# Performance work log

Hardware: AMD Instinct MI355X
Metric: run time of the kernel (lower is better)

The kernel has to match this reference:

```python
import jax, jax.numpy as jnp
import numpy as np

IN = 4096      # in_channels (unpacked)
OUT = 11008    # out_channels
GROUP = 128    # quantization group size
W_BIT = 4
PACK = 32 // W_BIT  # 8 int4 values per int32
N_GROUPS = IN // GROUP
BATCH = 64


def setup_inputs() -> dict:
    key = jax.random.key(0)
    k1, k2, k3, k4 = jax.random.split(key, 4)
    x = jax.random.normal(k1, (BATCH, IN), dtype=jnp.float32)
    # bit-packed int4 weights: 8 nibbles per int32, packed along input dim
    qweight = jax.random.randint(k2, (IN // PACK, OUT), 0, jnp.iinfo(jnp.int32).max, dtype=jnp.int32)
    scales = jax.random.uniform(k3, (N_GROUPS, OUT), dtype=jnp.float32) * 0.01 + 1e-3
    # zero points near mid-range of int4
    zeros = 7.5 + jax.random.uniform(k4, (N_GROUPS, OUT), dtype=jnp.float32) - 0.5
    g_idx = (jnp.arange(IN) // GROUP).astype(jnp.int32)
    return {"x": x, "qweight": qweight, "scales": scales, "zeros": zeros, "g_idx": g_idx}


def unpack_int4(qweight):
    # [IN//8, OUT] int32 -> [IN, OUT] float32 in [0, 15]
    shifts = (jnp.arange(PACK, dtype=jnp.int32) * W_BIT)  # [8]
    nibbles = (qweight[:, None, :] >> shifts[None, :, None]) & 0xF  # [IN//8, 8, OUT]
    return nibbles.reshape(IN, OUT).astype(jnp.float32)


def reference(x, qweight, scales, zeros, g_idx):
    w_int = unpack_int4(qweight)                       # [IN, OUT]
    W = (w_int - zeros[g_idx]) * scales[g_idx]         # group-wise dequant, [IN, OUT]
    return x @ W                                       # [BATCH, OUT]
```

## Files before the change

kernel.cpp:

```cpp
#include <hip/hip_runtime.h>
#include <stdint.h>


#define IN 4096
#define OUT 11008
#define BATCH 64
#define SPLITK 8
#define KSPL (IN / SPLITK)
#define BN 128
#define BK 64
#define NBLK (OUT / BN)
#define LDR 72

typedef __attribute__((ext_vector_type(8))) __bf16 bf16x8;
typedef __attribute__((ext_vector_type(4))) float f32x4;

static __device__ __forceinline__ ushort f2bf(float f) {
  uint32_t u = __float_as_uint(f);
  u += 0x7fff + ((u >> 16) & 1);
  return (ushort)(u >> 16);
}

__global__ void cvt_x_kernel(const float* __restrict__ x, ushort* __restrict__ xbf) {
  int gid = blockIdx.x * blockDim.x + threadIdx.x;
  float4 v = ((const float4*)x)[gid];
  ushort4 o;
  o.x = f2bf(v.x); o.y = f2bf(v.y); o.z = f2bf(v.z); o.w = f2bf(v.w);
  ((ushort4*)xbf)[gid] = o;
}

__global__ __launch_bounds__(256, 2) void mpq_gemm(
    const ushort* __restrict__ xbf,
    const int* __restrict__ qweight,
    const float* __restrict__ scales,
    const float* __restrict__ zeros,
    float* __restrict__ out)
{
  __shared__ ushort At[64 * LDR];
  __shared__ ushort Bt[128 * LDR];

  const int n0 = blockIdx.x * BN;
  const int k0 = blockIdx.y * KSPL;

  const int tid = threadIdx.x;
  const int lane = tid & 63;
  const int w = tid >> 6;
  const int wm = w >> 1, wn = w & 1;
  const int mlane = lane & 15, quad = lane >> 4;

  const int rA = tid >> 2;
  const int kA = (tid & 3) * 16;
  const int rB = tid >> 5;
  const int ncol = tid & 31;

  f32x4 acc[2][4] = {};

  for (int kc = k0; kc < k0 + KSPL; kc += BK) {
    const int g = kc >> 7;

    const uint4* asrc = (const uint4*)(xbf + rA * IN + kc + kA);
    uint4 a0 = asrc[0];
    uint4 a1 = asrc[1];

    int qv[4];
    float sv[4], zv[4];
    const int qrow = (kc >> 3) + rB;
#pragma unroll
    for (int c = 0; c < 4; ++c) {
      int n = ncol + 32 * c;
      qv[c] = qweight[qrow * OUT + n0 + n];
      sv[c] = scales[g * OUT + n0 + n];
      zv[c] = zeros[g * OUT + n0 + n];
    }

    __syncthreads();

    *(uint4*)&At[rA * LDR + kA] = a0;
    *(uint4*)&At[rA * LDR + kA + 8] = a1;

#pragma unroll
    for (int c = 0; c < 4; ++c) {
      const float s = sv[c];
      const float nzs = -zv[c] * s;
      const uint32_t q = (uint32_t)qv[c];
      ushort ob[8];
#pragma unroll
      for (int j = 0; j < 8; ++j) {
        float wf = (float)((q >> (4 * j)) & 0xF);
        ob[j] = f2bf(fmaf(wf, s, nzs));
      }
      *(uint4*)&Bt[(ncol + 32 * c) * LDR + rB * 8] = *(uint4*)ob;
    }

    __syncthreads();

#pragma unroll
    for (int ks = 0; ks < BK; ks += 32) {
      bf16x8 af[2], bfr[4];
#pragma unroll
      for (int i = 0; i < 2; ++i)
        af[i] = *(const bf16x8*)&At[(32 * wm + 16 * i + mlane) * LDR + ks + quad * 8];
#pragma unroll
      for (int j = 0; j < 4; ++j)
        bfr[j] = *(const bf16x8*)&Bt[(64 * wn + 16 * j + mlane) * LDR + ks + quad * 8];
#pragma unroll
      for (int i = 0; i < 2; ++i)
#pragma unroll
        for (int j = 0; j < 4; ++j)
          acc[i][j] = __builtin_amdgcn_mfma_f32_16x16x32_bf16(af[i], bfr[j], acc[i][j], 0, 0, 0);
    }
  }

#pragma unroll
  for (int i = 0; i < 2; ++i) {
    const int mbase = 32 * wm + 16 * i + quad * 4;
#pragma unroll
    for (int j = 0; j < 4; ++j) {
      const int col = n0 + 64 * wn + 16 * j + mlane;
#pragma unroll
      for (int r = 0; r < 4; ++r) {
        atomicAdd(&out[(mbase + r) * OUT + col], acc[i][j][r]);
      }
    }
  }
}

extern "C" void kernel_launch(void* const* d_in, const int* in_sizes, int n_in,
                              void* d_out, int out_size, void* d_ws, size_t ws_size,
                              hipStream_t stream) {
  const float* x = (const float*)d_in[0];
  const int* qweight = (const int*)d_in[1];
  const float* scales = (const float*)d_in[2];
  const float* zeros = (const float*)d_in[3];
  float* out = (float*)d_out;
  ushort* xbf = (ushort*)d_ws;

  hipMemsetAsync(d_out, 0, (size_t)BATCH * OUT * sizeof(float), stream);
  cvt_x_kernel<<<256, 256, 0, stream>>>(x, xbf);
  dim3 grid(NBLK, SPLITK);
  mpq_gemm<<<grid, 256, 0, stream>>>(xbf, qweight, scales, zeros, out);
}
```

Before: 106.0 us.

## Factor dequant out of MFMA via magic-number bf16 nibbles and group row sums

Rewrites the GEMM so int4 nibbles become bf16 directly through a 0x4300 magic-bias trick with no per-element float conversion or LDS staging of B. The per-group scale and zero are applied after the MFMAs, using precomputed per-group row sums of x, and results are folded into a running accumulator. x is pre-packed into MFMA fragment order, and the split-K atomics are replaced by per-split partial buffers plus a separate reduction kernel. This removes dequant ALU work and B shared-memory traffic, at the cost of an extra launch and extra partial-buffer write and read traffic.

```diff
diff --git a/kernel.cpp b/kernel.cpp
--- a/kernel.cpp
+++ b/kernel.cpp
@@ -6,11 +6,9 @@
 #define OUT 11008
 #define BATCH 64
 #define SPLITK 8
-#define KSPL (IN / SPLITK)
+#define KSPL 512
 #define BN 128
-#define BK 64
-#define NBLK (OUT / BN)
-#define LDR 72
+#define GRID_N 86
 
 typedef __attribute__((ext_vector_type(8))) __bf16 bf16x8;
 typedef __attribute__((ext_vector_type(4))) float f32x4;
@@ -20,109 +18,138 @@
   u += 0x7fff + ((u >> 16) & 1);
   return (ushort)(u >> 16);
 }
-
-__global__ void cvt_x_kernel(const float* __restrict__ x, ushort* __restrict__ xbf) {
-  int gid = blockIdx.x * blockDim.x + threadIdx.x;
-  float4 v = ((const float4*)x)[gid];
-  ushort4 o;
-  o.x = f2bf(v.x); o.y = f2bf(v.y); o.z = f2bf(v.z); o.w = f2bf(v.w);
-  ((ushort4*)xbf)[gid] = o;
+static __device__ __forceinline__ float bf2f(ushort h) {
+  return __uint_as_float(((uint32_t)h) << 16);
 }
 
-__global__ __launch_bounds__(256, 2) void mpq_gemm(
+__global__ void cvt_frag_kernel(const float* __restrict__ x,
+                                ushort* __restrict__ xbf,
+                                float* __restrict__ xsum) {
+  const int ks = blockIdx.x;
+  const int i = threadIdx.x >> 6;
+  const int lane = threadIdx.x & 63;
+  const int mlane = lane & 15, quad = lane >> 4;
+  const int m = 16 * i + mlane;
+  const int kb = 32 * ks + 8 * quad;
+  const float4 lo = *(const float4*)&x[m * IN + kb];
+  const float4 hi = *(const float4*)&x[m * IN + kb + 4];
+  ushort o[8];
+  o[0] = f2bf(lo.x); o[1] = f2bf(hi.x);
+  o[2] = f2bf(lo.y); o[3] = f2bf(hi.y);
+  o[4] = f2bf(lo.z); o[5] = f2bf(hi.z);
+  o[6] = f2bf(lo.w); o[7] = f2bf(hi.w);
+  const int flat = (ks * 4 + i) * 64 + lane;
+  *(uint4*)&xbf[flat * 8] = *(uint4*)o;
+  float s = 0.f;
+#pragma unroll
+  for (int j = 0; j < 8; ++j) s += bf2f(o[j]);
+  s += __shfl_xor(s, 16);
+  s += __shfl_xor(s, 32);
+  if (quad == 0) atomicAdd(&xsum[(ks >> 2) * 64 + m], s);
+}
+
+__global__ __launch_bounds__(128, 2) void mpq_gemm(
     const ushort* __restrict__ xbf,
     const int* __restrict__ qweight,
     const float* __restrict__ scales,
     const float* __restrict__ zeros,
-    float* __restrict__ out)
+    const float* __restrict__ xsum,
+    float* __restrict__ P)
 {
-  __shared__ ushort At[64 * LDR];
-  __shared__ ushort Bt[128 * LDR];
+  __shared__ uint4 A_lds[2048];
 
   const int n0 = blockIdx.x * BN;
-  const int k0 = blockIdx.y * KSPL;
-
+  const int sp = blockIdx.y;
+  const int k0 = sp * KSPL;
   const int tid = threadIdx.x;
   const int lane = tid & 63;
   const int w = tid >> 6;
-  const int wm = w >> 1, wn = w & 1;
   const int mlane = lane & 15, quad = lane >> 4;
+  const int ncol = n0 + 64 * w + mlane;
 
-  const int rA = tid >> 2;
-  const int kA = (tid & 3) * 16;
-  const int rB = tid >> 5;
-  const int ncol = tid & 31;
+  f32x4 macc[4][4] = {};
 
-  f32x4 acc[2][4] = {};
+  const uint4* gA = (const uint4*)xbf + (size_t)(k0 / 32) * 256;
 
-  for (int kc = k0; kc < k0 + KSPL; kc += BK) {
-    const int g = kc >> 7;
-
-    const uint4* asrc = (const uint4*)(xbf + rA * IN + kc + kA);
-    uint4 a0 = asrc[0];
-    uint4 a1 = asrc[1];
-
-    int qv[4];
-    float sv[4], zv[4];
-    const int qrow = (kc >> 3) + rB;
+  for (int h = 0; h < 2; ++h) {
+    __syncthreads();
+    const uint4* src = gA + (size_t)h * 8 * 256;
 #pragma unroll
-    for (int c = 0; c < 4; ++c) {
-      int n = ncol + 32 * c;
-      qv[c] = qweight[qrow * OUT + n0 + n];
-      sv[c] = scales[g * OUT + n0 + n];
-      zv[c] = zeros[g * OUT + n0 + n];
-    }
-
+    for (int it = 0; it < 16; ++it)
+      A_lds[tid + 128 * it] = src[tid + 128 * it];
     __syncthreads();
 
-    *(uint4*)&At[rA * LDR + kA] = a0;
-    *(uint4*)&At[rA * LDR + kA + 8] = a1;
-
+    const int qrow0 = k0 / 8 + h * 32;
 #pragma unroll
-    for (int c = 0; c < 4; ++c) {
-      const float s = sv[c];
-      const float nzs = -zv[c] * s;
-      const uint32_t q = (uint32_t)qv[c];
-      ushort ob[8];
+    for (int g2 = 0; g2 < 2; ++g2) {
+      f32x4 gacc[4][4] = {};
 #pragma unroll
-      for (int j = 0; j < 8; ++j) {
-        float wf = (float)((q >> (4 * j)) & 0xF);
-        ob[j] = f2bf(fmaf(wf, s, nzs));
-      }
-      *(uint4*)&Bt[(ncol + 32 * c) * LDR + rB * 8] = *(uint4*)ob;
-    }
-
-    __syncthreads();
-
-#pragma unroll
-    for (int ks = 0; ks < BK; ks += 32) {
-      bf16x8 af[2], bfr[4];
-#pragma unroll
-      for (int i = 0; i < 2; ++i)
-        af[i] = *(const bf16x8*)&At[(32 * wm + 16 * i + mlane) * LDR + ks + quad * 8];
-#pragma unroll
-      for (int j = 0; j < 4; ++j)
-        bfr[j] = *(const bf16x8*)&Bt[(64 * wn + 16 * j + mlane) * LDR + ks + quad * 8];
-#pragma unroll
-      for (int i = 0; i < 2; ++i)
+      for (int ksl = 0; ksl < 4; ++ksl) {
+        const int ks = g2 * 4 + ksl;
+        uint32_t q[4];
+        const int qrow = qrow0 + ks * 4 + quad;
 #pragma unroll
         for (int j = 0; j < 4; ++j)
-          acc[i][j] = __builtin_amdgcn_mfma_f32_16x16x32_bf16(af[i], bfr[j], acc[i][j], 0, 0, 0);
+          q[j] = (uint32_t)qweight[(size_t)qrow * OUT + ncol + 16 * j];
+        bf16x8 af[4];
+#pragma unroll
+        for (int i = 0; i < 4; ++i)
+          af[i] = *(const bf16x8*)&A_lds[(ks * 4 + i) * 64 + lane];
+#pragma unroll
+        for (int j = 0; j < 4; ++j) {
+          uint32_t p[4];
+          p[0] = ( q[j]        & 0x000F000Fu) | 0x43004300u;
+          p[1] = ((q[j] >>  4) & 0x000F000Fu) | 0x43004300u;
+          p[2] = ((q[j] >>  8) & 0x000F000Fu) | 0x43004300u;
+          p[3] = ((q[j] >> 12) & 0x000F000Fu) | 0x43004300u;
+          bf16x8 bfr = *(bf16x8*)p;
+#pragma unroll
+          for (int i = 0; i < 4; ++i)
+            gacc[i][j] = __builtin_amdgcn_mfma_f32_16x16x32_bf16(af[i], bfr, gacc[i][j], 0, 0, 0);
+        }
+      }
+      const int g = (k0 >> 7) + h * 2 + g2;
+      float Sv[4][4];
+#pragma unroll
+      for (int i = 0; i < 4; ++i)
+#pragma unroll
+        for (int r = 0; r < 4; ++r)
+          Sv[i][r] = xsum[g * 64 + 16 * i + 4 * quad + r];
+#pragma unroll
+      for (int j = 0; j < 4; ++j) {
+        const float s = scales[g * OUT + ncol + 16 * j];
+        const float z = zeros[g * OUT + ncol + 16 * j];
+        const float u = s * (128.0f + z);
+#pragma unroll
+        for (int i = 0; i < 4; ++i)
+#pragma unroll
+          for (int r = 0; r < 4; ++r)
+            macc[i][j][r] = fmaf(s, gacc[i][j][r], fmaf(-u, Sv[i][r], macc[i][j][r]));
+      }
     }
   }
 
+  float* Pp = P + (size_t)sp * BATCH * OUT;
 #pragma unroll
-  for (int i = 0; i < 2; ++i) {
-    const int mbase = 32 * wm + 16 * i + quad * 4;
+  for (int i = 0; i < 4; ++i)
 #pragma unroll
-    for (int j = 0; j < 4; ++j) {
-      const int col = n0 + 64 * wn + 16 * j + mlane;
+    for (int r = 0; r < 4; ++r) {
+      const int m = 16 * i + 4 * quad + r;
 #pragma unroll
-      for (int r = 0; r < 4; ++r) {
-        atomicAdd(&out[(mbase + r) * OUT + col], acc[i][j][r]);
-      }
+      for (int j = 0; j < 4; ++j)
+        Pp[(size_t)m * OUT + ncol + 16 * j] = macc[i][j][r];
     }
+}
+
+__global__ void reduce_kernel(const float* __restrict__ P, float* __restrict__ out) {
+  const int t = blockIdx.x * blockDim.x + threadIdx.x;
+  float4 a = ((const float4*)P)[t];
+#pragma unroll
+  for (int s = 1; s < SPLITK; ++s) {
+    float4 b = ((const float4*)P)[t + (size_t)s * (BATCH * OUT / 4)];
+    a.x += b.x; a.y += b.y; a.z += b.z; a.w += b.w;
   }
+  ((float4*)out)[t] = a;
 }
 
 extern "C" void kernel_launch(void* const* d_in, const int* in_sizes, int n_in,
@@ -134,9 +161,11 @@
   const float* zeros = (const float*)d_in[3];
   float* out = (float*)d_out;
   ushort* xbf = (ushort*)d_ws;
+  float* xsum = (float*)((char*)d_ws + (1 << 19));
+  float* P = (float*)((char*)d_ws + (1 << 20));
 
-  hipMemsetAsync(d_out, 0, (size_t)BATCH * OUT * sizeof(float), stream);
-  cvt_x_kernel<<<256, 256, 0, stream>>>(x, xbf);
-  dim3 grid(NBLK, SPLITK);
-  mpq_gemm<<<grid, 256, 0, stream>>>(xbf, qweight, scales, zeros, out);
+  hipMemsetAsync(xsum, 0, 32 * 64 * sizeof(float), stream);
+  cvt_frag_kernel<<<128, 256, 0, stream>>>(x, xbf, xsum);
+  mpq_gemm<<<dim3(GRID_N, SPLITK), 128, 0, stream>>>(xbf, qweight, scales, zeros, xsum, P);
+  reduce_kernel<<<BATCH * OUT / 4 / 256, 256, 0, stream>>>(P, out);
 }
```

Result: no change. 104.1 us (-1.8%).
